# Kernel optimization log

Hardware: AMD Instinct MI355X
Metric: run time of the kernel (lower is better)

Reference implementation:

```python
import jax, jax.numpy as jnp
import numpy as np

NUM_HEADS = 8
SR = 4
EPS = 1e-5


def _ln(x, w, b):
    mu = x.mean(-1, keepdims=True)
    var = ((x - mu) ** 2).mean(-1, keepdims=True)
    return (x - mu) / jnp.sqrt(var + EPS) * w + b


def _conv(x, w, b, stride, pad, groups):
    y = jax.lax.conv_general_dilated(
        x, w, (stride, stride), [(pad, pad), (pad, pad)],
        dimension_numbers=('NCHW', 'OIHW', 'NCHW'),
        feature_group_count=groups)
    return y + b[None, :, None, None]


def setup_inputs() -> dict:
    key = jax.random.key(0)
    ks = jax.random.split(key, 16)
    Q, B, C, H, W = 1024, 16, 512, 64, 64
    N = H * W
    C2 = C // 2
    f = jax.random.normal
    return {
        'query': f(ks[0], (Q, B, C), jnp.float32),
        'key': f(ks[1], (N, B, C), jnp.float32),
        'value': f(ks[2], (N, B, C), jnp.float32),
        'H': H, 'W': W,
        'q_w': f(ks[3], (C, C), jnp.float32) * 0.02,
        'sr1_w': f(ks[4], (C, C, 4, 4), jnp.float32) * 0.02,
        'sr1_b': jnp.zeros((C,), jnp.float32),
        'norm1_w': jnp.ones((C,), jnp.float32),
        'norm1_b': jnp.zeros((C,), jnp.float32),
        'sr2_w': f(ks[5], (C, C, 2, 2), jnp.float32) * 0.02,
        'sr2_b': jnp.zeros((C,), jnp.float32),
        'norm2_w': jnp.ones((C,), jnp.float32),
        'norm2_b': jnp.zeros((C,), jnp.float32),
        'k1_w': f(ks[6], (C2, C), jnp.float32) * 0.02,
        'v1_w': f(ks[7], (C2, C), jnp.float32) * 0.02,
        'k2_w': f(ks[8], (C2, C), jnp.float32) * 0.02,
        'v2_w': f(ks[9], (C2, C), jnp.float32) * 0.02,
        'lc1_w': f(ks[10], (C2, 1, 3, 3), jnp.float32) * 0.2,
        'lc1_b': jnp.zeros((C2,), jnp.float32),
        'lc2_w': f(ks[11], (C2, 1, 3, 3), jnp.float32) * 0.2,
        'lc2_b': jnp.zeros((C2,), jnp.float32),
        'proj_w': f(ks[12], (C, C), jnp.float32) * 0.02,
        'proj_b': jnp.zeros((C,), jnp.float32),
    }


def reference(query, key, value, H, W, q_w, sr1_w, sr1_b, norm1_w, norm1_b,
              sr2_w, sr2_b, norm2_w, norm2_b, k1_w, v1_w, k2_w, v2_w,
              lc1_w, lc1_b, lc2_w, lc2_b, proj_w, proj_b):
    Qn, B, C = query.shape
    nh2 = NUM_HEADS // 2
    hd = C // NUM_HEADS
    C2 = C // 2
    scale = hd ** -0.5
    gelu = lambda t: jax.nn.gelu(t, approximate=False)

    # NOTE: original does reshape(B, Q, nh, hd) on a (Q,B,C) tensor -- raw reshape, kept faithful.
    q = (query @ q_w.T).reshape(B, Qn, NUM_HEADS, hd).transpose(0, 2, 1, 3)  # (B,nh,Q,hd)

    key_ = key.transpose(0, 2, 1).reshape(B, C, H, W)
    value_ = value.transpose(0, 2, 1).reshape(B, C, H, W)

    def sr_branch(x, w, b, stride, nw, nb):
        y = _conv(x, w, b, stride, 0, 1).reshape(B, C, -1).transpose(0, 2, 1)
        return gelu(_ln(y, nw, nb))

    key_1 = sr_branch(key_, sr1_w, sr1_b, SR, norm1_w, norm1_b)        # (B,N1,C)
    value_1 = sr_branch(value_, sr1_w, sr1_b, SR, norm1_w, norm1_b)
    key_2 = sr_branch(key_, sr2_w, sr2_b, SR // 2, norm2_w, norm2_b)   # (B,N2,C)
    value_2 = sr_branch(value_, sr2_w, sr2_b, SR // 2, norm2_w, norm2_b)

    def heads(x, w):  # (B,N,C) -> (B,nh2,N,hd)
        return (x @ w.T).reshape(B, -1, nh2, hd).transpose(0, 2, 1, 3)

    k1 = heads(key_1, k1_w)
    v1 = heads(value_1, k1_w)  # faithful: source uses self.k1(value_1)
    k2 = heads(key_2, k2_w)
    v2 = heads(value_2, v2_w)

    h1, w1 = H // SR, W // SR
    h2, w2 = H * 2 // SR, W * 2 // SR

    def local_res(v, lw, lb, hh, ww):
        Nn = v.shape[2]
        img = v.transpose(0, 2, 1, 3).reshape(B, Nn, C2).transpose(0, 2, 1).reshape(B, C2, hh, ww)
        lc = _conv(img, lw, lb, 1, 1, C2).reshape(B, nh2, hd, Nn).transpose(0, 1, 3, 2)
        return v + lc

    attn1 = jax.nn.softmax(jnp.einsum('bhqd,bhkd->bhqk', q[:, :nh2], k1) * scale, axis=-1)
    v1 = local_res(v1, lc1_w, lc1_b, h1, w1)
    x1 = jnp.einsum('bhqk,bhkd->bhqd', attn1, v1).transpose(0, 2, 1, 3).reshape(B, Qn, C2)

    attn2 = jax.nn.softmax(jnp.einsum('bhqd,bhkd->bhqk', q[:, nh2:], k2) * scale, axis=-1)
    v2 = local_res(v2, lc2_w, lc2_b, h2, w2)
    x2 = jnp.einsum('bhqk,bhkd->bhqd', attn2, v2).transpose(0, 2, 1, 3).reshape(B, Qn, C2)

    x = jnp.concatenate([x1, x2], axis=-1)
    return x @ proj_w.T + proj_b
```

## Files before the change

### kernel.cpp

```cpp
#include <hip/hip_runtime.h>
#include <hip/hip_bf16.h>
#include <math.h>

using bf16 = __hip_bfloat16;

typedef __bf16 bf16x4 __attribute__((ext_vector_type(4)));
typedef __bf16 bf16x8 __attribute__((ext_vector_type(8)));
typedef float  floatx4 __attribute__((ext_vector_type(4)));

__device__ __forceinline__ float b2f(bf16 x) { return __bfloat162float(x); }
__device__ __forceinline__ bf16  f2b(float x) { return __float2bfloat16(x); }

__device__ __forceinline__ int swz(int i) { return i ^ (((i >> 11) & 15) << 2); }

struct DcEnt { const float* s; __bf16* d; int n; };
struct DcPack { DcEnt e[8]; };

__global__ void __launch_bounds__(256)
downcast_all(DcPack p, int n_ent)
{
    const int ei = blockIdx.y;
    if (ei >= n_ent) return;
    const DcEnt ent = p.e[ei];
    const int i4 = (blockIdx.x * 256 + threadIdx.x) * 4;
    if (i4 + 3 >= ent.n) {
        for (int i = i4; i < ent.n; ++i) ent.d[i] = (__bf16)ent.s[i];
        return;
    }
    float4 v = *(const float4*)(ent.s + i4);
    bf16x4 o = { (__bf16)v.x, (__bf16)v.y, (__bf16)v.z, (__bf16)v.w };
    *(bf16x4*)(ent.d + i4) = o;
}

__global__ void __launch_bounds__(256)
im2col_sr1(const float* __restrict__ src, __bf16* __restrict__ dst)
{
    __shared__ __bf16 lds[8192];
    const int b  = blockIdx.x >> 8;
    const int c2 = blockIdx.x & 255;
    const int tid = threadIdx.x;
    const float* sp = src + ((size_t)(b * 256 + c2) << 13);

#pragma unroll
    for (int i = 0; i < 8; ++i) {
        int idx = (i * 256 + tid) * 4;
        float4 v = *(const float4*)(sp + idx);
        int o = swz(idx);
        lds[o + 0] = (__bf16)v.x; lds[o + 1] = (__bf16)v.y;
        lds[o + 2] = (__bf16)v.z; lds[o + 3] = (__bf16)v.w;
    }
    __syncthreads();

    const int j = tid & 3;
#pragma unroll
    for (int p = 0; p < 4; ++p) {
        int r  = p * 64 + (tid >> 2);
        int oy = r >> 4, ox = r & 15;
        bf16x8 o;
#pragma unroll
        for (int u = 0; u < 8; ++u) {
            int e  = j * 8 + u;
            int cc = e >> 4, ky = (e >> 2) & 3, kx = e & 3;
            int i  = (4 * (ox & 3) + kx) * 512 + cc * 256 +
                     (4 * oy + ky) * 4 + (ox >> 2);
            o[u] = lds[swz(i)];
        }
        *(bf16x8*)(dst + ((size_t)(b * 256 + r) << 13) + c2 * 32 + j * 8) = o;
    }
}

__global__ void __launch_bounds__(256)
im2col_sr2(const float* __restrict__ src, __bf16* __restrict__ dst)
{
    __shared__ __bf16 lds[32768];
    const int b  = blockIdx.x >> 6;
    const int cg = blockIdx.x & 63;
    const int tid = threadIdx.x;
    const float* sp = src + ((size_t)(b * 256 + cg * 4) << 13);

#pragma unroll
    for (int i = 0; i < 32; ++i) {
        int idx = (i * 256 + tid) * 4;
        float4 v = *(const float4*)(sp + idx);
        int o = swz(idx);
        lds[o + 0] = (__bf16)v.x; lds[o + 1] = (__bf16)v.y;
        lds[o + 2] = (__bf16)v.z; lds[o + 3] = (__bf16)v.w;
    }
    __syncthreads();

    const int j = tid & 3;
#pragma unroll
    for (int p = 0; p < 16; ++p) {
        int r  = p * 64 + (tid >> 2);
        int oy = r >> 5, ox = r & 31;
        bf16x8 o;
#pragma unroll
        for (int u = 0; u < 8; ++u) {
            int cc = (u >> 2) & 1, ky = (u >> 1) & 1, kx = u & 1;
            int i  = j * 8192 + (2 * (ox & 7) + kx) * 512 + cc * 256 +
                     (2 * oy + ky) * 4 + (ox >> 3);
            o[u] = lds[swz(i)];
        }
        *(bf16x8*)(dst + ((size_t)(b * 1024 + r) << 11) + cg * 32 + j * 8) = o;
    }
}

template <int BN, typename OutT>
__global__ void __launch_bounds__(256)
mgemm(const __bf16* __restrict__ A, const __bf16* __restrict__ B,
      const float* __restrict__ bias, OutT* __restrict__ C,
      int N, int K)
{
    constexpr int BM = 128, BK = 64;
    constexpr int PK = BK + 8;
    constexpr int NI = BN / 32;
    __shared__ __bf16 Asl[BM * PK];
    __shared__ __bf16 Bsl[BN * PK];

    const int tid  = threadIdx.x;
    const int w    = tid >> 6, lane = tid & 63;
    const int quad = lane >> 4, l16 = lane & 15;
    const int wm   = (w >> 1) * 64, wn = (w & 1) * (BN / 2);
    const int m0   = blockIdx.x * BM, n0 = blockIdx.y * BN;

    floatx4 acc[4][NI];
#pragma unroll
    for (int mi = 0; mi < 4; ++mi)
#pragma unroll
        for (int ni = 0; ni < NI; ++ni)
            acc[mi][ni] = (floatx4){0.f, 0.f, 0.f, 0.f};

    for (int k0 = 0; k0 < K; k0 += BK) {
#pragma unroll
        for (int i = 0; i < (BM * BK / 8) / 256; ++i) {
            int idx = (i * 256 + tid) * 8;
            int m = idx >> 6, kk = idx & 63;
            *(bf16x8*)&Asl[m * PK + kk] =
                *(const bf16x8*)&A[(size_t)(m0 + m) * K + k0 + kk];
        }
#pragma unroll
        for (int i = 0; i < (BN * BK / 8) / 256; ++i) {
            int idx = (i * 256 + tid) * 8;
            int n = idx >> 6, kk = idx & 63;
            *(bf16x8*)&Bsl[n * PK + kk] =
                *(const bf16x8*)&B[(size_t)(n0 + n) * K + k0 + kk];
        }
        __syncthreads();
#pragma unroll
        for (int ks = 0; ks < 2; ++ks) {
            bf16x8 af[4], bf[NI];
#pragma unroll
            for (int mi = 0; mi < 4; ++mi)
                af[mi] = *(const bf16x8*)&Asl[(wm + mi * 16 + l16) * PK + ks * 32 + quad * 8];
#pragma unroll
            for (int ni = 0; ni < NI; ++ni)
                bf[ni] = *(const bf16x8*)&Bsl[(wn + ni * 16 + l16) * PK + ks * 32 + quad * 8];
#pragma unroll
            for (int mi = 0; mi < 4; ++mi)
#pragma unroll
                for (int ni = 0; ni < NI; ++ni)
                    acc[mi][ni] = __builtin_amdgcn_mfma_f32_16x16x32_bf16(
                        af[mi], bf[ni], acc[mi][ni], 0, 0, 0);
        }
        __syncthreads();
    }

#pragma unroll
    for (int mi = 0; mi < 4; ++mi)
#pragma unroll
        for (int r = 0; r < 4; ++r) {
            int row = m0 + wm + mi * 16 + quad * 4 + r;
#pragma unroll
            for (int ni = 0; ni < NI; ++ni) {
                int col = n0 + wn + ni * 16 + l16;
                float v = acc[mi][ni][r];
                if (bias) v += bias[col];
                C[(size_t)row * N + col] = (OutT)v;
            }
        }
}

template <int BN>
__global__ void __launch_bounds__(256)
mgemm_sk(const __bf16* __restrict__ A, const __bf16* __restrict__ B,
         float* __restrict__ P, int N, int K, int KC, size_t mn)
{
    constexpr int BM = 128, BK = 64;
    constexpr int PK = BK + 8;
    constexpr int NI = BN / 32;
    __shared__ __bf16 Asl[BM * PK];
    __shared__ __bf16 Bsl[BN * PK];

    const int tid  = threadIdx.x;
    const int w    = tid >> 6, lane = tid & 63;
    const int quad = lane >> 4, l16 = lane & 15;
    const int wm   = (w >> 1) * 64, wn = (w & 1) * (BN / 2);
    const int m0   = blockIdx.x * BM, n0 = blockIdx.y * BN;
    const int kbeg = blockIdx.z * KC;

    floatx4 acc[4][NI];
#pragma unroll
    for (int mi = 0; mi < 4; ++mi)
#pragma unroll
        for (int ni = 0; ni < NI; ++ni)
            acc[mi][ni] = (floatx4){0.f, 0.f, 0.f, 0.f};

    for (int k0 = kbeg; k0 < kbeg + KC; k0 += BK) {
#pragma unroll
        for (int i = 0; i < (BM * BK / 8) / 256; ++i) {
            int idx = (i * 256 + tid) * 8;
            int m = idx >> 6, kk = idx & 63;
            *(bf16x8*)&Asl[m * PK + kk] =
                *(const bf16x8*)&A[(size_t)(m0 + m) * K + k0 + kk];
        }
#pragma unroll
        for (int i = 0; i < (BN * BK / 8) / 256; ++i) {
            int idx = (i * 256 + tid) * 8;
            int n = idx >> 6, kk = idx & 63;
            *(bf16x8*)&Bsl[n * PK + kk] =
                *(const bf16x8*)&B[(size_t)(n0 + n) * K + k0 + kk];
        }
        __syncthreads();
#pragma unroll
        for (int ks = 0; ks < 2; ++ks) {
            bf16x8 af[4], bf[NI];
#pragma unroll
            for (int mi = 0; mi < 4; ++mi)
                af[mi] = *(const bf16x8*)&Asl[(wm + mi * 16 + l16) * PK + ks * 32 + quad * 8];
#pragma unroll
            for (int ni = 0; ni < NI; ++ni)
                bf[ni] = *(const bf16x8*)&Bsl[(wn + ni * 16 + l16) * PK + ks * 32 + quad * 8];
#pragma unroll
            for (int mi = 0; mi < 4; ++mi)
#pragma unroll
                for (int ni = 0; ni < NI; ++ni)
                    acc[mi][ni] = __builtin_amdgcn_mfma_f32_16x16x32_bf16(
                        af[mi], bf[ni], acc[mi][ni], 0, 0, 0);
        }
        __syncthreads();
    }

    float* Pz = P + (size_t)blockIdx.z * mn;
#pragma unroll
    for (int mi = 0; mi < 4; ++mi)
#pragma unroll
        for (int r = 0; r < 4; ++r) {
            int row = m0 + wm + mi * 16 + quad * 4 + r;
#pragma unroll
            for (int ni = 0; ni < NI; ++ni) {
                int col = n0 + wn + ni * 16 + l16;
                Pz[(size_t)row * N + col] = acc[mi][ni][r];
            }
        }
}

__global__ void __launch_bounds__(256)
sk_reduce(const float* __restrict__ P, const float* __restrict__ bias,
          __bf16* __restrict__ out, size_t mn, int nsplit, int nmask)
{
    const size_t i = ((size_t)blockIdx.x * 256 + threadIdx.x) * 4;
    if (i >= mn) return;
    float4 s = *(const float4*)(P + i);
    for (int z = 1; z < nsplit; ++z) {
        float4 t = *(const float4*)(P + (size_t)z * mn + i);
        s.x += t.x; s.y += t.y; s.z += t.z; s.w += t.w;
    }
    if (bias) {
        const int c = (int)(i & (size_t)nmask);
        s.x += bias[c]; s.y += bias[c + 1]; s.z += bias[c + 2]; s.w += bias[c + 3];
    }
    bf16x4 o = { (__bf16)s.x, (__bf16)s.y, (__bf16)s.z, (__bf16)s.w };
    *(bf16x4*)(out + i) = o;
}

__global__ void __launch_bounds__(256)
ln_gelu(bf16* __restrict__ data, const float* __restrict__ w, const float* __restrict__ bp)
{
    __shared__ float red[256];
    const int tid = threadIdx.x;
    const size_t base = (size_t)blockIdx.x * 512;
    float x0 = b2f(data[base + tid]);
    float x1 = b2f(data[base + 256 + tid]);

    red[tid] = x0 + x1;
    __syncthreads();
#pragma unroll
    for (int off = 128; off > 0; off >>= 1) {
        if (tid < off) red[tid] += red[tid + off];
        __syncthreads();
    }
    float mu = red[0] * (1.0f / 512.0f);
    __syncthreads();

    float d0 = x0 - mu, d1 = x1 - mu;
    red[tid] = d0 * d0 + d1 * d1;
    __syncthreads();
#pragma unroll
    for (int off = 128; off > 0; off >>= 1) {
        if (tid < off) red[tid] += red[tid + off];
        __syncthreads();
    }
    float rstd = rsqrtf(red[0] * (1.0f / 512.0f) + 1e-5f);

    float y0 = d0 * rstd * w[tid] + bp[tid];
    float y1 = d1 * rstd * w[256 + tid] + bp[256 + tid];
    y0 = 0.5f * y0 * (1.0f + erff(y0 * 0.70710678118654752f));
    y1 = 0.5f * y1 * (1.0f + erff(y1 * 0.70710678118654752f));
    data[base + tid]       = f2b(y0);
    data[base + 256 + tid] = f2b(y1);
}

__global__ void __launch_bounds__(256)
local_res(const bf16* __restrict__ v, const float* __restrict__ lw,
          const float* __restrict__ lb, bf16* __restrict__ outp,
          int hw_bits, int w1_bits)
{
    const int idx = blockIdx.x * 256 + threadIdx.x;
    const int c   = idx & 255;
    const int pix = (idx >> 8) & ((1 << hw_bits) - 1);
    const int b   = idx >> (8 + hw_bits);
    const int w1  = 1 << w1_bits;
    const int h1  = 1 << (hw_bits - w1_bits);
    const int y = pix >> w1_bits, x = pix & (w1 - 1);

    float acc = b2f(v[idx]) + lb[c];
#pragma unroll
    for (int ky = 0; ky < 3; ++ky) {
        int yy = y + ky - 1;
        if (yy < 0 || yy >= h1) continue;
#pragma unroll
        for (int kx = 0; kx < 3; ++kx) {
            int xx = x + kx - 1;
            if (xx < 0 || xx >= w1) continue;
            acc += lw[c * 9 + ky * 3 + kx] *
                   b2f(v[(((b << hw_bits) + (yy << w1_bits) + xx) << 8) + c]);
        }
    }
    outp[idx] = f2b(acc);
}

__global__ void __launch_bounds__(256)
attn_mfma(const bf16* __restrict__ qmat, const bf16* __restrict__ kmat,
          const bf16* __restrict__ vmat, bf16* __restrict__ x,
          int Nk, int hoff, int xoff)
{
    __shared__ __bf16 lds_vt[64][40];
    __shared__ __bf16 lds_p[4][16][40];

    const int bid = blockIdx.x;
    const int qt = bid & 15;
    const int h  = (bid >> 4) & 3;
    const int b  = bid >> 6;
    const int tid = threadIdx.x;
    const int w = tid >> 6, lane = tid & 63;
    const int quad = lane >> 4, l16 = lane & 15;

    const int qrow = b * 1024 + qt * 64 + w * 16 + l16;
    const __bf16* qp = (const __bf16*)qmat + (size_t)qrow * 512 + (hoff + h) * 64 + quad * 8;
    const bf16x8 qf0 = *(const bf16x8*)qp;
    const bf16x8 qf1 = *(const bf16x8*)(qp + 32);

    floatx4 acc_o[4];
#pragma unroll
    for (int nt = 0; nt < 4; ++nt) acc_o[nt] = (floatx4){0.f, 0.f, 0.f, 0.f};
    float rs[4] = {0.f, 0.f, 0.f, 0.f};

    const size_t kvbase = (size_t)b * Nk * 256 + (size_t)h * 64;

    for (int j0 = 0; j0 < Nk; j0 += 32) {
        __syncthreads();
        {
            const int jr = tid >> 3;
            const int dc = (tid & 7) * 8;
            bf16x8 vv = *(const bf16x8*)((const __bf16*)vmat + kvbase +
                                         (size_t)(j0 + jr) * 256 + dc);
#pragma unroll
            for (int e = 0; e < 8; ++e)
                lds_vt[dc + e][jr] = vv[e];
        }
        __syncthreads();

#pragma unroll
        for (int jh = 0; jh < 2; ++jh) {
            const __bf16* kp = (const __bf16*)kmat + kvbase +
                               (size_t)(j0 + jh * 16 + l16) * 256 + quad * 8;
            bf16x8 kf0 = *(const bf16x8*)kp;
            bf16x8 kf1 = *(const bf16x8*)(kp + 32);
            floatx4 s = (floatx4){0.f, 0.f, 0.f, 0.f};
            s = __builtin_amdgcn_mfma_f32_16x16x32_bf16(qf0, kf0, s, 0, 0, 0);
            s = __builtin_amdgcn_mfma_f32_16x16x32_bf16(qf1, kf1, s, 0, 0, 0);
#pragma unroll
            for (int r = 0; r < 4; ++r) {
                float p = __expf(s[r] * 0.125f);
                rs[r] += p;
                lds_p[w][quad * 4 + r][jh * 16 + l16] = (__bf16)p;
            }
        }
        bf16x8 pf = *(const bf16x8*)&lds_p[w][l16][quad * 8];
#pragma unroll
        for (int nt = 0; nt < 4; ++nt) {
            bf16x8 vf = *(const bf16x8*)&lds_vt[nt * 16 + l16][quad * 8];
            acc_o[nt] = __builtin_amdgcn_mfma_f32_16x16x32_bf16(pf, vf, acc_o[nt], 0, 0, 0);
        }
    }

#pragma unroll
    for (int r = 0; r < 4; ++r) {
        float v = rs[r];
        v += __shfl_xor(v, 1);
        v += __shfl_xor(v, 2);
        v += __shfl_xor(v, 4);
        v += __shfl_xor(v, 8);
        rs[r] = v;
    }

    const int mg = qt * 64 + w * 16 + quad * 4;
#pragma unroll
    for (int r = 0; r < 4; ++r) {
        const float inv = 1.0f / rs[r];
        __bf16* xr = (__bf16*)x + (size_t)(b * 1024 + mg + r) * 512 + xoff + h * 64;
#pragma unroll
        for (int nt = 0; nt < 4; ++nt)
            xr[nt * 16 + l16] = (__bf16)(acc_o[nt][r] * inv);
    }
}

extern "C" void kernel_launch(void* const* d_in, const int* in_sizes, int n_in,
                              void* d_out, int out_size, void* d_ws, size_t ws_size,
                              hipStream_t stream)
{
    const float* query   = (const float*)d_in[0];
    const float* key     = (const float*)d_in[1];
    const float* value   = (const float*)d_in[2];
    const float* q_w     = (const float*)d_in[5];
    const float* sr1_w   = (const float*)d_in[6];
    const float* sr1_b   = (const float*)d_in[7];
    const float* norm1_w = (const float*)d_in[8];
    const float* norm1_b = (const float*)d_in[9];
    const float* sr2_w   = (const float*)d_in[10];
    const float* sr2_b   = (const float*)d_in[11];
    const float* norm2_w = (const float*)d_in[12];
    const float* norm2_b = (const float*)d_in[13];
    const float* k1_w    = (const float*)d_in[14];
    const float* k2_w    = (const float*)d_in[16];
    const float* v2_w    = (const float*)d_in[17];
    const float* lc1_w   = (const float*)d_in[18];
    const float* lc1_b   = (const float*)d_in[19];
    const float* lc2_w   = (const float*)d_in[20];
    const float* lc2_b   = (const float*)d_in[21];
    const float* proj_w  = (const float*)d_in[22];
    const float* proj_b  = (const float*)d_in[23];
    float* out = (float*)d_out;

    char* base = (char*)d_ws;
    const size_t MiB = 1024 * 1024;
    __bf16* S     = (__bf16*)(base + 0 * MiB);
    __bf16* qproj = S;
    __bf16* k1    = (__bf16*)(base + 16 * MiB);
    __bf16* v1    = (__bf16*)(base + 18 * MiB);
    __bf16* k2    = (__bf16*)(base + 20 * MiB);
    __bf16* v2    = (__bf16*)(base + 28 * MiB);
    __bf16* qbf   = (__bf16*)(base + 36 * MiB);
    __bf16* c1k   = (__bf16*)(base + 64 * MiB);
    __bf16* c1v   = (__bf16*)(base + 68 * MiB);
    __bf16* c2k   = (__bf16*)(base + 72 * MiB);
    __bf16* c2v   = (__bf16*)(base + 88 * MiB);
    float*  skp   = (float*)(base + 72 * MiB);
    __bf16* wq    = (__bf16*)(base + 104 * MiB);
    __bf16* wsr1  = (__bf16*)(base + 104 * MiB + 524288);
    __bf16* wsr2  = (__bf16*)(base + 112 * MiB + 524288);
    __bf16* wk1   = (__bf16*)(base + 114 * MiB + 524288);
    __bf16* wk2   = (__bf16*)(base + 114 * MiB + 786432);
    __bf16* wv2   = (__bf16*)(base + 115 * MiB);
    __bf16* wproj = (__bf16*)(base + 115 * MiB + 262144);
    __bf16* v1r   = c1k;
    __bf16* v2r   = c2v;
    __bf16* xbuf  = c2k;

    dim3 blk(256);

    {
        DcPack p;
        p.e[0] = { q_w,    wq,    512 * 512 };
        p.e[1] = { sr1_w,  wsr1,  512 * 8192 };
        p.e[2] = { sr2_w,  wsr2,  512 * 2048 };
        p.e[3] = { k1_w,   wk1,   256 * 512 };
        p.e[4] = { k2_w,   wk2,   256 * 512 };
        p.e[5] = { v2_w,   wv2,   256 * 512 };
        p.e[6] = { proj_w, wproj, 512 * 512 };
        p.e[7] = { nullptr, nullptr, 0 };
        int maxb = (512 * 8192 / 4 + 255) / 256;
        downcast_all<<<dim3(maxb, 7), blk, 0, stream>>>(p, 7);
    }

    const size_t mn1 = 4096 * 512;
    im2col_sr1<<<dim3(4096), blk, 0, stream>>>(key, S);
    mgemm_sk<64><<<dim3(32, 8, 4), blk, 0, stream>>>(S, wsr1, skp, 512, 8192, 2048, mn1);
    sk_reduce<<<dim3(mn1 / 1024), blk, 0, stream>>>(skp, sr1_b, c1k, mn1, 4, 511);
    im2col_sr1<<<dim3(4096), blk, 0, stream>>>(value, S);
    mgemm_sk<64><<<dim3(32, 8, 4), blk, 0, stream>>>(S, wsr1, skp, 512, 8192, 2048, mn1);
    sk_reduce<<<dim3(mn1 / 1024), blk, 0, stream>>>(skp, sr1_b, c1v, mn1, 4, 511);
    im2col_sr2<<<dim3(1024), blk, 0, stream>>>(key, S);
    mgemm<64, __bf16><<<dim3(128, 8), blk, 0, stream>>>(S, wsr2, sr2_b, c2k, 512, 2048);
    im2col_sr2<<<dim3(1024), blk, 0, stream>>>(value, S);
    mgemm<64, __bf16><<<dim3(128, 8), blk, 0, stream>>>(S, wsr2, sr2_b, c2v, 512, 2048);

    {
        DcPack p;
        p.e[0] = { query, qbf, 16384 * 512 };
        downcast_all<<<dim3(16384 * 512 / 1024, 1), blk, 0, stream>>>(p, 1);
    }
    mgemm<64, __bf16><<<dim3(128, 8), blk, 0, stream>>>(qbf, wq, nullptr, qproj, 512, 512);

    ln_gelu<<<dim3(4096),  blk, 0, stream>>>((bf16*)c1k, norm1_w, norm1_b);
    ln_gelu<<<dim3(4096),  blk, 0, stream>>>((bf16*)c1v, norm1_w, norm1_b);
    ln_gelu<<<dim3(16384), blk, 0, stream>>>((bf16*)c2k, norm2_w, norm2_b);
    ln_gelu<<<dim3(16384), blk, 0, stream>>>((bf16*)c2v, norm2_w, norm2_b);

    mgemm<64, __bf16><<<dim3(32, 4),  blk, 0, stream>>>(c1k, wk1, nullptr, k1, 256, 512);
    mgemm<64, __bf16><<<dim3(32, 4),  blk, 0, stream>>>(c1v, wk1, nullptr, v1, 256, 512);
    mgemm<64, __bf16><<<dim3(128, 4), blk, 0, stream>>>(c2k, wk2, nullptr, k2, 256, 512);
    mgemm<64, __bf16><<<dim3(128, 4), blk, 0, stream>>>(c2v, wv2, nullptr, v2, 256, 512);

    local_res<<<dim3(4096),  blk, 0, stream>>>((bf16*)v1, lc1_w, lc1_b, (bf16*)v1r, 8, 4);
    local_res<<<dim3(16384), blk, 0, stream>>>((bf16*)v2, lc2_w, lc2_b, (bf16*)v2r, 10, 5);

    attn_mfma<<<dim3(1024), blk, 0, stream>>>((bf16*)qproj, (bf16*)k1, (bf16*)v1r,
                                              (bf16*)xbuf, 256, 0, 0);
    attn_mfma<<<dim3(1024), blk, 0, stream>>>((bf16*)qproj, (bf16*)k2, (bf16*)v2r,
                                              (bf16*)xbuf, 1024, 4, 256);

    mgemm<64, float><<<dim3(128, 8), blk, 0, stream>>>(xbuf, wproj, proj_b, out, 512, 512);
}
```

Measured before the change: 1.021 ms.

## Pre-transpose V, stage K in LDS, and register-prefetch next K/V tile in attention

```diff
diff --git a/kernel.cpp b/kernel.cpp
--- a/kernel.cpp
+++ b/kernel.cpp
@@ -340,10 +340,44 @@
 }
 
 __global__ void __launch_bounds__(256)
+vtrans(const __bf16* __restrict__ in, __bf16* __restrict__ out, int Nk)
+{
+    __shared__ __bf16 t[64][72];
+    const int jt = blockIdx.x, cg = blockIdx.y, b = blockIdx.z;
+    const int tid = threadIdx.x;
+    const int chunk = tid & 7;
+
+#pragma unroll
+    for (int i = 0; i < 2; ++i) {
+        int jr = i * 32 + (tid >> 3);
+        bf16x8 v = *(const bf16x8*)(in + ((size_t)(b * Nk + jt * 64 + jr) << 8)
+                                       + cg * 64 + chunk * 8);
+        int ch = chunk ^ ((jr >> 3) & 7);
+        *(bf16x8*)&t[jr][ch * 8] = v;
+    }
+    __syncthreads();
+
+#pragma unroll
+    for (int i = 0; i < 2; ++i) {
+        int cr = i * 32 + (tid >> 3);
+        int jc = tid & 7;
+        bf16x8 o;
+#pragma unroll
+        for (int u = 0; u < 8; ++u) {
+            int j  = jc * 8 + u;
+            int ch = (cr >> 3) ^ ((j >> 3) & 7);
+            o[u] = t[j][ch * 8 + (cr & 7)];
+        }
+        *(bf16x8*)(out + (size_t)(b * 256 + cg * 64 + cr) * Nk + jt * 64 + jc * 8) = o;
+    }
+}
+
+__global__ void __launch_bounds__(256)
 attn_mfma(const bf16* __restrict__ qmat, const bf16* __restrict__ kmat,
-          const bf16* __restrict__ vmat, bf16* __restrict__ x,
+          const bf16* __restrict__ vtmat, bf16* __restrict__ x,
           int Nk, int hoff, int xoff)
 {
+    __shared__ __bf16 lds_k[32][72];
     __shared__ __bf16 lds_vt[64][40];
     __shared__ __bf16 lds_p[4][16][40];
 
@@ -360,30 +394,32 @@
     const bf16x8 qf0 = *(const bf16x8*)qp;
     const bf16x8 qf1 = *(const bf16x8*)(qp + 32);
 
+    const __bf16* ksrc = (const __bf16*)kmat + ((size_t)b * Nk << 8)
+                         + (size_t)(tid >> 3) * 256 + h * 64 + (tid & 7) * 8;
+    const __bf16* vsrc = (const __bf16*)vtmat
+                         + (size_t)(b * 256 + h * 64 + (tid >> 2)) * Nk + (tid & 3) * 8;
+
+    bf16x8 kreg = *(const bf16x8*)ksrc;
+    bf16x8 vreg = *(const bf16x8*)vsrc;
+
     floatx4 acc_o[4];
 #pragma unroll
     for (int nt = 0; nt < 4; ++nt) acc_o[nt] = (floatx4){0.f, 0.f, 0.f, 0.f};
     float rs[4] = {0.f, 0.f, 0.f, 0.f};
 
-    const size_t kvbase = (size_t)b * Nk * 256 + (size_t)h * 64;
-
     for (int j0 = 0; j0 < Nk; j0 += 32) {
         __syncthreads();
-        {
-            const int jr = tid >> 3;
-            const int dc = (tid & 7) * 8;
-            bf16x8 vv = *(const bf16x8*)((const __bf16*)vmat + kvbase +
-                                         (size_t)(j0 + jr) * 256 + dc);
-#pragma unroll
-            for (int e = 0; e < 8; ++e)
-                lds_vt[dc + e][jr] = vv[e];
-        }
-        __syncthreads();
+        *(bf16x8*)&lds_k[tid >> 3][(tid & 7) * 8] = kreg;
+        *(bf16x8*)&lds_vt[tid >> 2][(tid & 3) * 8] = vreg;
+        __syncthreads();
+        if (j0 + 32 < Nk) {
+            kreg = *(const bf16x8*)(ksrc + ((size_t)(j0 + 32) << 8));
+            vreg = *(const bf16x8*)(vsrc + j0 + 32);
+        }
 
 #pragma unroll
         for (int jh = 0; jh < 2; ++jh) {
-            const __bf16* kp = (const __bf16*)kmat + kvbase +
-                               (size_t)(j0 + jh * 16 + l16) * 256 + quad * 8;
+            const __bf16* kp = &lds_k[jh * 16 + l16][quad * 8];
             bf16x8 kf0 = *(const bf16x8*)kp;
             bf16x8 kf1 = *(const bf16x8*)(kp + 32);
             floatx4 s = (floatx4){0.f, 0.f, 0.f, 0.f};
@@ -461,6 +497,8 @@
     __bf16* k2    = (__bf16*)(base + 20 * MiB);
     __bf16* v2    = (__bf16*)(base + 28 * MiB);
     __bf16* qbf   = (__bf16*)(base + 36 * MiB);
+    __bf16* vt2   = (__bf16*)(base + 36 * MiB);
+    __bf16* vt1   = (__bf16*)(base + 44 * MiB);
     __bf16* c1k   = (__bf16*)(base + 64 * MiB);
     __bf16* c1v   = (__bf16*)(base + 68 * MiB);
     __bf16* c2k   = (__bf16*)(base + 72 * MiB);
@@ -524,10 +562,12 @@
 
     local_res<<<dim3(4096),  blk, 0, stream>>>((bf16*)v1, lc1_w, lc1_b, (bf16*)v1r, 8, 4);
     local_res<<<dim3(16384), blk, 0, stream>>>((bf16*)v2, lc2_w, lc2_b, (bf16*)v2r, 10, 5);
-
-    attn_mfma<<<dim3(1024), blk, 0, stream>>>((bf16*)qproj, (bf16*)k1, (bf16*)v1r,
+    vtrans<<<dim3(4, 4, 16),  blk, 0, stream>>>(v1r, vt1, 256);
+    vtrans<<<dim3(16, 4, 16), blk, 0, stream>>>(v2r, vt2, 1024);
+
+    attn_mfma<<<dim3(1024), blk, 0, stream>>>((bf16*)qproj, (bf16*)k1, (bf16*)vt1,
                                               (bf16*)xbuf, 256, 0, 0);
-    attn_mfma<<<dim3(1024), blk, 0, stream>>>((bf16*)qproj, (bf16*)k2, (bf16*)v2r,
+    attn_mfma<<<dim3(1024), blk, 0, stream>>>((bf16*)qproj, (bf16*)k2, (bf16*)vt2,
                                               (bf16*)xbuf, 1024, 4, 256);
 
     mgemm<64, float><<<dim3(128, 8), blk, 0, stream>>>(xbuf, wproj, proj_b, out, 512, 512);
```

Measured after the change: 953.9 us. -6.6%, faster.
